# Optimization experiments

Hardware: AMD Instinct MI355X
Metric: run time of the kernel (lower is better)

The kernel has to match this reference:

```python
import jax, jax.numpy as jnp
import numpy as np

EPS = 1e-5

def layer_norm(x, gamma, beta):
    mu = jnp.mean(x, axis=-1, keepdims=True)
    var = jnp.mean(jnp.square(x - mu), axis=-1, keepdims=True)
    return (x - mu) * jax.lax.rsqrt(var + EPS) * gamma + beta

def setup_inputs() -> dict:
    key = jax.random.key(0)
    ks = jax.random.split(key, 12)
    B, N, F, H, K = 32, 2048, 128, 256, 64
    A_hat = jax.random.uniform(ks[0], (B, N, N), dtype=jnp.float32) / N  # row-normalized-ish adjacency
    X = jax.random.normal(ks[1], (B, N, F), dtype=jnp.float32)
    def lin(k, din, dout):
        s = 1.0 / np.sqrt(din)
        k1, k2 = jax.random.split(k)
        W = jax.random.uniform(k1, (din, dout), minval=-s, maxval=s, dtype=jnp.float32)
        b = jax.random.uniform(k2, (dout,), minval=-s, maxval=s, dtype=jnp.float32)
        return W, b
    W1, b1 = lin(ks[2], F, H)
    W2, b2 = lin(ks[3], H, H)
    Wa, ba = lin(ks[4], H, K)
    Wl, bl = lin(ks[5], H, K)
    g1 = jnp.ones((H,), jnp.float32); beta1 = jnp.zeros((H,), jnp.float32)
    g2 = jnp.ones((H,), jnp.float32); beta2 = jnp.zeros((H,), jnp.float32)
    return {"A_hat": A_hat, "X": X, "W1": W1, "b1": b1, "g1": g1, "beta1": beta1,
            "W2": W2, "b2": b2, "g2": g2, "beta2": beta2,
            "Wa": Wa, "ba": ba, "Wl": Wl, "bl": bl}

def reference(A_hat, X, W1, b1, g1, beta1, W2, b2, g2, beta2, Wa, ba, Wl, bl):
    # Layer 1: aggregate -> linear -> LayerNorm -> ReLU (dropout is eval identity)
    H = jnp.einsum('bnm,bmf->bnf', A_hat, X)
    H = jnp.einsum('bnf,fh->bnh', H, W1) + b1
    H = jax.nn.relu(layer_norm(H, g1, beta1))
    # Layer 2
    H = jnp.einsum('bnm,bmh->bnh', A_hat, H)
    H = jnp.einsum('bnh,hk->bnk', H, W2) + b2
    H = jax.nn.relu(layer_norm(H, g2, beta2))
    # mean readout over nodes
    g = jnp.mean(H, axis=1)
    pred_arr_reg = g @ Wa + ba
    logits = g @ Wl + bl
    return (pred_arr_reg, logits)
```

## Files before the change

kernel.cpp:

```cpp
#include <hip/hip_runtime.h>
#include <hip/hip_bf16.h>

#define NN 2048

typedef __attribute__((ext_vector_type(4))) float f32x4;
typedef __attribute__((ext_vector_type(8))) short bf16x8;

__device__ __forceinline__ unsigned short f2bf(float f) {
  __hip_bfloat16 h = __float2bfloat16(f);
  return __builtin_bit_cast(unsigned short, h);
}
__device__ __forceinline__ unsigned int pk2(float a, float b) {
  return (unsigned int)f2bf(a) | ((unsigned int)f2bf(b) << 16);
}
__device__ __forceinline__ void gld_lds16(const void* g, void* l) {
  __builtin_amdgcn_global_load_lds(
      (const __attribute__((address_space(1))) unsigned int*)g,
      (__attribute__((address_space(3))) unsigned int*)l, 16, 0, 0);
}

__global__ void k_tr_cvt(const float* __restrict__ src, unsigned short* __restrict__ dst,
                         int R, int C) {
  int b = blockIdx.z;
  src += (size_t)b * R * C;
  dst += (size_t)b * R * C;
  __shared__ float tile[32][33];
  int r0 = blockIdx.x * 32, c0 = blockIdx.y * 32;
  int t = threadIdx.x;
  int r = t >> 3, c4 = (t & 7) << 2;
  float4 v = *(const float4*)(src + (size_t)(r0 + r) * C + c0 + c4);
  tile[r][c4 + 0] = v.x; tile[r][c4 + 1] = v.y; tile[r][c4 + 2] = v.z; tile[r][c4 + 3] = v.w;
  __syncthreads();
  ushort4 o;
  o.x = f2bf(tile[c4 + 0][r]); o.y = f2bf(tile[c4 + 1][r]);
  o.z = f2bf(tile[c4 + 2][r]); o.w = f2bf(tile[c4 + 3][r]);
  *(ushort4*)(dst + (size_t)(c0 + r) * R + r0 + c4) = o;
}

#define AGG_STEP(KT, AREGC, AREGN, CUR)                                        \
  {                                                                            \
    const int kt_ = (KT);                                                      \
    if (kt_ < NKT - 2) {                 \
      const float* p_ = apb + (size_t)(kt_ + 2) * 64;                          \
      _Pragma("unroll") for (int j = 0; j < F4; ++j)                           \
          AREGN[j] = ((const float4*)p_)[j];                                   \
    }                                                                          \
    if (kt_ < NKT - 1) {                                                       \
      _Pragma("unroll") for (int i = 0; i < 4; ++i) {         \
        int jj = i * NT + t;                                                   \
        int n_ = jj >> 3, s_ = jj & 7, sp_ = s_ ^ (n_ & 7);                    \
        gld_lds16(BTb + (size_t)n_ * NN + (size_t)(kt_ + 1) * 64 + sp_ * 8,    \
                  &Bs[(CUR) ^ 1][(i * NT + wid * 64) * 8]);                    \
      }                                                                        \
      _Pragma("unroll") for (int i = 0; i < F4 / 2; ++i) {  \
        uint4 w_;                                                              \
        w_.x = pk2(AREGC[2 * i].x, AREGC[2 * i].y);                            \
        w_.y = pk2(AREGC[2 * i].z, AREGC[2 * i].w);                            \
        w_.z = pk2(AREGC[2 * i + 1].x, AREGC[2 * i + 1].y);                    \
        w_.w = pk2(AREGC[2 * i + 1].z, AREGC[2 * i + 1].w);                    \
        int s_ = ak * (F4 / 2) + i, sp_ = s_ ^ (ar & 7);                       \
        *(uint4*)&As[(CUR) ^ 1][(ar * 8 + sp_) * 8] = w_;                      \
      }                                                                        \
    }                                                                          \
    _Pragma("unroll") for (int kh = 0; kh < 2; ++kh) {                         \
      bf16x8 af[4], bfr[4];                                                    \
      _Pragma("unroll") for (int mi = 0; mi < 4; ++mi) {                       \
        int row = wr * 64 + mi * 16 + lr;                                      \
        int sp_ = (kh * 4 + q) ^ (row & 7);                                    \
        af[mi] = *(const bf16x8*)&As[CUR][(row * 8 + sp_) * 8];                \
      }                                                                        \
      _Pragma("unroll") for (int ni = 0; ni < 4; ++ni) {                       \
        int row = wc * 64 + ni * 16 + lr;                                      \
        int sp_ = (kh * 4 + q) ^ (row & 7);                                    \
        bfr[ni] = *(const bf16x8*)&Bs[CUR][(row * 8 + sp_) * 8];               \
      }                                                                        \
      _Pragma("unroll") for (int mi = 0; mi < 4; ++mi)                         \
        _Pragma("unroll") for (int ni = 0; ni < 4; ++ni)                       \
          acc[mi][ni] = __builtin_amdgcn_mfma_f32_16x16x32_bf16(               \
              af[mi], bfr[ni], acc[mi][ni], 0, 0, 0);                          \
    }                                                                          \
    __syncthreads();                                                           \
  }

template <int NCOLS>
__global__ __launch_bounds__(NCOLS * 2, 2) void k_agg(
    const float* __restrict__ A, const unsigned short* __restrict__ BT,
    unsigned short* __restrict__ C) {
  constexpr int NT = NCOLS * 2;
  constexpr int NWC = NCOLS / 64;
  constexpr int TPR = NT / 128;
  constexpr int FPT = 8192 / NT;
  constexpr int F4 = FPT / 4;
  constexpr int NKT = NN / 64;
  static_assert(NCOLS * 8 == NT * 4, "B gld count");

  __shared__ __align__(16) unsigned short As[2][128 * 64];
  __shared__ __align__(16) unsigned short Bs[2][NCOLS * 64];
  int b = blockIdx.z;
  const float* Ab = A + (size_t)b * NN * NN;
  const unsigned short* BTb = BT + (size_t)b * (size_t)NCOLS * NN;
  unsigned short* Cb = C + (size_t)b * NN * NCOLS;
  int m0 = blockIdx.x * 128;
  int t = threadIdx.x, lane = t & 63, wid = t >> 6;
  int wr = wid / NWC, wc = wid % NWC;
  int q = lane >> 4, lr = lane & 15;
  int ar = t / TPR, ak = t % TPR;
  const float* apb = Ab + (size_t)(m0 + ar) * NN + ak * FPT;

  f32x4 acc[4][4] = {};
  float4 aregA[F4], aregB[F4];

  {
#pragma unroll
    for (int j = 0; j < F4; ++j) aregA[j] = ((const float4*)apb)[j];
#pragma unroll
    for (int i = 0; i < 4; ++i) {
      int jj = i * NT + t;
      int n = jj >> 3, s = jj & 7, sp = s ^ (n & 7);
      gld_lds16(BTb + (size_t)n * NN + sp * 8, &Bs[0][(i * NT + wid * 64) * 8]);
    }
#pragma unroll
    for (int i = 0; i < F4 / 2; ++i) {
      uint4 w;
      w.x = pk2(aregA[2 * i].x, aregA[2 * i].y);
      w.y = pk2(aregA[2 * i].z, aregA[2 * i].w);
      w.z = pk2(aregA[2 * i + 1].x, aregA[2 * i + 1].y);
      w.w = pk2(aregA[2 * i + 1].z, aregA[2 * i + 1].w);
      int s = ak * (F4 / 2) + i, sp = s ^ (ar & 7);
      *(uint4*)&As[0][(ar * 8 + sp) * 8] = w;
    }
#pragma unroll
    for (int j = 0; j < F4; ++j) aregB[j] = ((const float4*)(apb + 64))[j];
  }
  __syncthreads();

  for (int k2 = 0; k2 < NKT / 2; ++k2) {
    AGG_STEP(2 * k2, aregB, aregA, 0);
    AGG_STEP(2 * k2 + 1, aregA, aregB, 1);
  }

#pragma unroll
  for (int mi = 0; mi < 4; ++mi) {
#pragma unroll
    for (int ni = 0; ni < 4; ++ni) {
#pragma unroll
      for (int j = 0; j < 4; ++j) {
        int row = m0 + wr * 64 + mi * 16 + q * 4 + j;
        int col = wc * 64 + ni * 16 + lr;
        Cb[(size_t)row * NCOLS + col] = f2bf(acc[mi][ni][j]);
      }
    }
  }
}

__global__ void k_lin_ln(const unsigned short* __restrict__ Hin, const unsigned short* __restrict__ WT,
                         const float* __restrict__ bias, const float* __restrict__ gamma,
                         const float* __restrict__ beta, int Fin,
                         unsigned short* __restrict__ HTout, float* __restrict__ gpart, int mode) {
  __shared__ __align__(16) unsigned short Ash[128 * 64];
  __shared__ __align__(16) unsigned short Wsh[256 * 64];
  __shared__ float red[2][128][4];
  int b = blockIdx.y, n0 = blockIdx.x * 128;
  const unsigned short* Hb = Hin + (size_t)b * NN * Fin;
  int t = threadIdx.x, lane = t & 63, wid = t >> 6;
  int wr = wid >> 2, wc = wid & 3;
  int q = lane >> 4, lr = lane & 15;
  f32x4 acc[4][4] = {};
  int nkt = Fin >> 6;
  for (int kt = 0; kt < nkt; ++kt) {
#pragma unroll
    for (int i = 0; i < 2; ++i) {
      int jj = i * 512 + t;
      int n = jj >> 3, s = jj & 7, sp = s ^ (n & 7);
      gld_lds16(Hb + (size_t)(n0 + n) * Fin + kt * 64 + sp * 8, &Ash[(i * 512 + wid * 64) * 8]);
    }
#pragma unroll
    for (int i = 0; i < 4; ++i) {
      int jj = i * 512 + t;
      int h = jj >> 3, s = jj & 7, sp = s ^ (h & 7);
      gld_lds16(WT + (size_t)h * Fin + kt * 64 + sp * 8, &Wsh[(i * 512 + wid * 64) * 8]);
    }
    __syncthreads();
#pragma unroll
    for (int kh = 0; kh < 2; ++kh) {
      bf16x8 af[4], wf[4];
#pragma unroll
      for (int mi = 0; mi < 4; ++mi) {
        int row = wr * 64 + mi * 16 + lr;
        int sp = (kh * 4 + q) ^ (row & 7);
        af[mi] = *(const bf16x8*)&Ash[(row * 8 + sp) * 8];
      }
#pragma unroll
      for (int ni = 0; ni < 4; ++ni) {
        int hrow = wc * 64 + ni * 16 + lr;
        int sp = (kh * 4 + q) ^ (hrow & 7);
        wf[ni] = *(const bf16x8*)&Wsh[(hrow * 8 + sp) * 8];
      }
#pragma unroll
      for (int mi = 0; mi < 4; ++mi) {
#pragma unroll
        for (int ni = 0; ni < 4; ++ni)
          acc[mi][ni] = __builtin_amdgcn_mfma_f32_16x16x32_bf16(af[mi], wf[ni], acc[mi][ni], 0, 0, 0);
      }
    }
    __syncthreads();
  }
  float bcol[4], gcol[4], zcol[4];
#pragma unroll
  for (int ni = 0; ni < 4; ++ni) {
    int col = wc * 64 + ni * 16 + lr;
    bcol[ni] = bias[col]; gcol[ni] = gamma[col]; zcol[ni] = beta[col];
  }
#pragma unroll
  for (int mi = 0; mi < 4; ++mi) {
#pragma unroll
    for (int j = 0; j < 4; ++j) {
      float s = 0.f, ss = 0.f;
#pragma unroll
      for (int ni = 0; ni < 4; ++ni) {
        float v = acc[mi][ni][j] + bcol[ni];
        acc[mi][ni][j] = v;
        s += v; ss += v * v;
      }
#pragma unroll
      for (int m = 1; m < 16; m <<= 1) { s += __shfl_xor(s, m); ss += __shfl_xor(ss, m); }
      if (lr == 0) {
        int rl = wr * 64 + mi * 16 + q * 4 + j;
        red[0][rl][wc] = s;
        red[1][rl][wc] = ss;
      }
    }
  }
  __syncthreads();
#pragma unroll
  for (int mi = 0; mi < 4; ++mi) {
#pragma unroll
    for (int j = 0; j < 4; ++j) {
      int rl = wr * 64 + mi * 16 + q * 4 + j;
      float s = red[0][rl][0] + red[0][rl][1] + red[0][rl][2] + red[0][rl][3];
      float ss = red[1][rl][0] + red[1][rl][1] + red[1][rl][2] + red[1][rl][3];
      float mean = s * (1.f / 256.f);
      float var = ss * (1.f / 256.f) - mean * mean;
      float inv = rsqrtf(var + 1e-5f);
#pragma unroll
      for (int ni = 0; ni < 4; ++ni) {
        float v = (acc[mi][ni][j] - mean) * inv * gcol[ni] + zcol[ni];
        acc[mi][ni][j] = v > 0.f ? v : 0.f;
      }
    }
  }
  if (mode == 0) {
#pragma unroll
    for (int mi = 0; mi < 4; ++mi) {
#pragma unroll
      for (int ni = 0; ni < 4; ++ni) {
        int col = wc * 64 + ni * 16 + lr;
        int rowb = n0 + wr * 64 + mi * 16 + q * 4;
        ushort4 o;
        o.x = f2bf(acc[mi][ni][0]); o.y = f2bf(acc[mi][ni][1]);
        o.z = f2bf(acc[mi][ni][2]); o.w = f2bf(acc[mi][ni][3]);
        *(ushort4*)(HTout + ((size_t)b * 256 + col) * NN + rowb) = o;
      }
    }
  } else {
#pragma unroll
    for (int ni = 0; ni < 4; ++ni) {
      float cs = 0.f;
#pragma unroll
      for (int mi = 0; mi < 4; ++mi) {
#pragma unroll
        for (int j = 0; j < 4; ++j) cs += acc[mi][ni][j];
      }
      cs += __shfl_xor(cs, 16);
      cs += __shfl_xor(cs, 32);
      if (q == 0) {
        int col = wc * 64 + ni * 16 + lr;
        gpart[(((size_t)b * 16 + blockIdx.x) * 2 + wr) * 256 + col] = cs;
      }
    }
  }
}

__global__ void k_readout(const float* __restrict__ gpart, const float* __restrict__ Wa,
                          const float* __restrict__ ba, const float* __restrict__ Wl,
                          const float* __restrict__ bl, float* __restrict__ out) {
  __shared__ float gl[256];
  int b = blockIdx.x, t = threadIdx.x;
  float s = 0.f;
#pragma unroll 4
  for (int p = 0; p < 32; ++p) s += gpart[((size_t)b * 32 + p) * 256 + t];
  gl[t] = s * (1.f / 2048.f);
  __syncthreads();
  if (t < 128) {
    int k = t & 63;
    const float* W = (t >= 64) ? Wl : Wa;
    const float* bb = (t >= 64) ? bl : ba;
    float a = 0.f;
    for (int h = 0; h < 256; ++h) a += gl[h] * W[h * 64 + k];
    a += bb[k];
    out[((t >= 64) ? 2048 : 0) + b * 64 + k] = a;
  }
}

extern "C" void kernel_launch(void* const* d_in, const int* in_sizes, int n_in,
                              void* d_out, int out_size, void* d_ws, size_t ws_size,
                              hipStream_t stream) {
  const float* A_hat = (const float*)d_in[0];
  const float* X   = (const float*)d_in[1];
  const float* W1  = (const float*)d_in[2];
  const float* b1  = (const float*)d_in[3];
  const float* g1  = (const float*)d_in[4];
  const float* be1 = (const float*)d_in[5];
  const float* W2  = (const float*)d_in[6];
  const float* b2  = (const float*)d_in[7];
  const float* g2  = (const float*)d_in[8];
  const float* be2 = (const float*)d_in[9];
  const float* Wa  = (const float*)d_in[10];
  const float* ba  = (const float*)d_in[11];
  const float* Wl  = (const float*)d_in[12];
  const float* bl  = (const float*)d_in[13];

  char* ws = (char*)d_ws;
  const size_t MB = 1024 * 1024;
  unsigned short* XT    = (unsigned short*)(ws);
  unsigned short* Hagg1 = (unsigned short*)(ws + 16 * MB);
  unsigned short* Hagg2 = (unsigned short*)(ws);
  unsigned short* H1T   = (unsigned short*)(ws + 32 * MB);
  unsigned short* W1T   = (unsigned short*)(ws + 64 * MB);
  unsigned short* W2T   = (unsigned short*)(ws + 64 * MB + 256 * 1024);
  float* gpart          = (float*)(ws + 65 * MB);

  k_tr_cvt<<<dim3(64, 4, 32), 256, 0, stream>>>(X, XT, 2048, 128);
  k_tr_cvt<<<dim3(4, 8, 1), 256, 0, stream>>>(W1, W1T, 128, 256);
  k_tr_cvt<<<dim3(8, 8, 1), 256, 0, stream>>>(W2, W2T, 256, 256);
  k_agg<128><<<dim3(16, 1, 32), 256, 0, stream>>>(A_hat, XT, Hagg1);
  k_lin_ln<<<dim3(16, 32), 512, 0, stream>>>(Hagg1, W1T, b1, g1, be1, 128, H1T, nullptr, 0);
  k_agg<256><<<dim3(16, 1, 32), 512, 0, stream>>>(A_hat, H1T, Hagg2);
  k_lin_ln<<<dim3(16, 32), 512, 0, stream>>>(Hagg2, W2T, b2, g2, be2, 256, nullptr, gpart, 1);
  k_readout<<<dim3(32), 256, 0, stream>>>(gpart, Wa, ba, Wl, bl, (float*)d_out);
}
```

Before: 390.0 us.

## Fuse aggregation GEMM with linear+LayerNorm+ReLU epilogue in one kernel

Merges k_agg and k_lin_ln into one templated kernel. Each block keeps its aggregated 128-row tile in LDS as bf16, reusing the A/B staging buffers, then runs the weight GEMM, LayerNorm and ReLU directly on it. This removes the global round trip of the intermediate Hagg buffers and two kernel launches. The layer-1 aggregation also moves from 256 to 512 threads with a different warp tiling, trading register and occupancy behaviour for the fusion.

```diff
diff --git a/kernel.cpp b/kernel.cpp
--- a/kernel.cpp
+++ b/kernel.cpp
@@ -40,97 +40,98 @@
 #define AGG_STEP(KT, AREGC, AREGN, CUR)                                        \
   {                                                                            \
     const int kt_ = (KT);                                                      \
-    if (kt_ < NKT - 2) {                 \
+    if (kt_ < NKT - 2) {                           \
       const float* p_ = apb + (size_t)(kt_ + 2) * 64;                          \
-      _Pragma("unroll") for (int j = 0; j < F4; ++j)                           \
+      _Pragma("unroll") for (int j = 0; j < 4; ++j)                            \
           AREGN[j] = ((const float4*)p_)[j];                                   \
     }                                                                          \
     if (kt_ < NKT - 1) {                                                       \
-      _Pragma("unroll") for (int i = 0; i < 4; ++i) {         \
-        int jj = i * NT + t;                                                   \
+      _Pragma("unroll") for (int i = 0; i < NF; ++i) {        \
+        int jj = i * 512 + t;                                                  \
         int n_ = jj >> 3, s_ = jj & 7, sp_ = s_ ^ (n_ & 7);                    \
         gld_lds16(BTb + (size_t)n_ * NN + (size_t)(kt_ + 1) * 64 + sp_ * 8,    \
-                  &Bs[(CUR) ^ 1][(i * NT + wid * 64) * 8]);                    \
+                  &Bs[(CUR) ^ 1][(i * 512 + wid * 64) * 8]);                   \
       }                                                                        \
-      _Pragma("unroll") for (int i = 0; i < F4 / 2; ++i) {  \
+      _Pragma("unroll") for (int i = 0; i < 2; ++i) {     \
         uint4 w_;                                                              \
         w_.x = pk2(AREGC[2 * i].x, AREGC[2 * i].y);                            \
         w_.y = pk2(AREGC[2 * i].z, AREGC[2 * i].w);                            \
         w_.z = pk2(AREGC[2 * i + 1].x, AREGC[2 * i + 1].y);                    \
         w_.w = pk2(AREGC[2 * i + 1].z, AREGC[2 * i + 1].w);                    \
-        int s_ = ak * (F4 / 2) + i, sp_ = s_ ^ (ar & 7);                       \
+        int s_ = ak * 2 + i, sp_ = s_ ^ (ar & 7);                              \
         *(uint4*)&As[(CUR) ^ 1][(ar * 8 + sp_) * 8] = w_;                      \
       }                                                                        \
     }                                                                          \
     _Pragma("unroll") for (int kh = 0; kh < 2; ++kh) {                         \
-      bf16x8 af[4], bfr[4];                                                    \
+      bf16x8 af[4], bfr[NF];                                                   \
       _Pragma("unroll") for (int mi = 0; mi < 4; ++mi) {                       \
         int row = wr * 64 + mi * 16 + lr;                                      \
         int sp_ = (kh * 4 + q) ^ (row & 7);                                    \
         af[mi] = *(const bf16x8*)&As[CUR][(row * 8 + sp_) * 8];                \
       }                                                                        \
-      _Pragma("unroll") for (int ni = 0; ni < 4; ++ni) {                       \
-        int row = wc * 64 + ni * 16 + lr;                                      \
-        int sp_ = (kh * 4 + q) ^ (row & 7);                                    \
-        bfr[ni] = *(const bf16x8*)&Bs[CUR][(row * 8 + sp_) * 8];               \
+      _Pragma("unroll") for (int ni = 0; ni < NF; ++ni) {                      \
+        int brow = wc * WN + ni * 16 + lr;                                     \
+        int sp_ = (kh * 4 + q) ^ (brow & 7);                                   \
+        bfr[ni] = *(const bf16x8*)&Bs[CUR][(brow * 8 + sp_) * 8];              \
       }                                                                        \
       _Pragma("unroll") for (int mi = 0; mi < 4; ++mi)                         \
-        _Pragma("unroll") for (int ni = 0; ni < 4; ++ni)                       \
+        _Pragma("unroll") for (int ni = 0; ni < NF; ++ni)                      \
           acc[mi][ni] = __builtin_amdgcn_mfma_f32_16x16x32_bf16(               \
               af[mi], bfr[ni], acc[mi][ni], 0, 0, 0);                          \
     }                                                                          \
     __syncthreads();                                                           \
   }
 
-template <int NCOLS>
-__global__ __launch_bounds__(NCOLS * 2, 2) void k_agg(
+template <int NCOLS, int MODE>
+__global__ __launch_bounds__(512, NCOLS == 128 ? 4 : 2) void k_agg_fused(
     const float* __restrict__ A, const unsigned short* __restrict__ BT,
-    unsigned short* __restrict__ C) {
-  constexpr int NT = NCOLS * 2;
-  constexpr int NWC = NCOLS / 64;
-  constexpr int TPR = NT / 128;
-  constexpr int FPT = 8192 / NT;
-  constexpr int F4 = FPT / 4;
+    const unsigned short* __restrict__ WT, const float* __restrict__ bias,
+    const float* __restrict__ gamma, const float* __restrict__ beta,
+    unsigned short* __restrict__ HTout, float* __restrict__ gpart) {
+  constexpr int WN = NCOLS / 4;
+  constexpr int NF = NCOLS / 64;
   constexpr int NKT = NN / 64;
-  static_assert(NCOLS * 8 == NT * 4, "B gld count");
+  constexpr int FIN = NCOLS;
+  constexpr int NQT = FIN / 64;
 
   __shared__ __align__(16) unsigned short As[2][128 * 64];
   __shared__ __align__(16) unsigned short Bs[2][NCOLS * 64];
+  __shared__ float red[2][128][4];
+
   int b = blockIdx.z;
   const float* Ab = A + (size_t)b * NN * NN;
   const unsigned short* BTb = BT + (size_t)b * (size_t)NCOLS * NN;
-  unsigned short* Cb = C + (size_t)b * NN * NCOLS;
   int m0 = blockIdx.x * 128;
   int t = threadIdx.x, lane = t & 63, wid = t >> 6;
-  int wr = wid / NWC, wc = wid % NWC;
+  int wr = wid >> 2, wc = wid & 3;
   int q = lane >> 4, lr = lane & 15;
-  int ar = t / TPR, ak = t % TPR;
-  const float* apb = Ab + (size_t)(m0 + ar) * NN + ak * FPT;
-
-  f32x4 acc[4][4] = {};
-  float4 aregA[F4], aregB[F4];
+  int ar = t >> 2, ak = t & 3;
+  const float* apb = Ab + (size_t)(m0 + ar) * NN + ak * 16;
+
+  f32x4 acc[4][NF] = {};
+  float4 aregA[4], aregB[4];
 
   {
 #pragma unroll
-    for (int j = 0; j < F4; ++j) aregA[j] = ((const float4*)apb)[j];
-#pragma unroll
-    for (int i = 0; i < 4; ++i) {
-      int jj = i * NT + t;
+    for (int j = 0; j < 4; ++j) aregA[j] = ((const float4*)apb)[j];
+#pragma unroll
+    for (int i = 0; i < NF; ++i) {
+      int jj = i * 512 + t;
       int n = jj >> 3, s = jj & 7, sp = s ^ (n & 7);
-      gld_lds16(BTb + (size_t)n * NN + sp * 8, &Bs[0][(i * NT + wid * 64) * 8]);
-    }
-#pragma unroll
-    for (int i = 0; i < F4 / 2; ++i) {
+      gld_lds16(BTb + (size_t)n * NN + sp * 8, &Bs[0][(i * 512 + wid * 64) * 8]);
+    }
+#pragma unroll
+    for (int i = 0; i < 2; ++i) {
       uint4 w;
       w.x = pk2(aregA[2 * i].x, aregA[2 * i].y);
       w.y = pk2(aregA[2 * i].z, aregA[2 * i].w);
       w.z = pk2(aregA[2 * i + 1].x, aregA[2 * i + 1].y);
       w.w = pk2(aregA[2 * i + 1].z, aregA[2 * i + 1].w);
-      int s = ak * (F4 / 2) + i, sp = s ^ (ar & 7);
+      int s = ak * 2 + i, sp = s ^ (ar & 7);
       *(uint4*)&As[0][(ar * 8 + sp) * 8] = w;
     }
 #pragma unroll
-    for (int j = 0; j < F4; ++j) aregB[j] = ((const float4*)(apb + 64))[j];
+    for (int j = 0; j < 4; ++j) aregB[j] = ((const float4*)(apb + 64))[j];
   }
   __syncthreads();
 
@@ -139,72 +140,57 @@
     AGG_STEP(2 * k2 + 1, aregA, aregB, 1);
   }
 
+  unsigned short* Hs = (NCOLS == 128) ? &As[0][0] : &Bs[0][0];
+  unsigned short* Ws = (NCOLS == 128) ? &Bs[0][0] : &As[0][0];
 #pragma unroll
   for (int mi = 0; mi < 4; ++mi) {
 #pragma unroll
-    for (int ni = 0; ni < 4; ++ni) {
+    for (int ni = 0; ni < NF; ++ni) {
 #pragma unroll
       for (int j = 0; j < 4; ++j) {
-        int row = m0 + wr * 64 + mi * 16 + q * 4 + j;
-        int col = wc * 64 + ni * 16 + lr;
-        Cb[(size_t)row * NCOLS + col] = f2bf(acc[mi][ni][j]);
-      }
-    }
-  }
-}
-
-__global__ void k_lin_ln(const unsigned short* __restrict__ Hin, const unsigned short* __restrict__ WT,
-                         const float* __restrict__ bias, const float* __restrict__ gamma,
-                         const float* __restrict__ beta, int Fin,
-                         unsigned short* __restrict__ HTout, float* __restrict__ gpart, int mode) {
-  __shared__ __align__(16) unsigned short Ash[128 * 64];
-  __shared__ __align__(16) unsigned short Wsh[256 * 64];
-  __shared__ float red[2][128][4];
-  int b = blockIdx.y, n0 = blockIdx.x * 128;
-  const unsigned short* Hb = Hin + (size_t)b * NN * Fin;
-  int t = threadIdx.x, lane = t & 63, wid = t >> 6;
-  int wr = wid >> 2, wc = wid & 3;
-  int q = lane >> 4, lr = lane & 15;
-  f32x4 acc[4][4] = {};
-  int nkt = Fin >> 6;
-  for (int kt = 0; kt < nkt; ++kt) {
-#pragma unroll
-    for (int i = 0; i < 2; ++i) {
-      int jj = i * 512 + t;
-      int n = jj >> 3, s = jj & 7, sp = s ^ (n & 7);
-      gld_lds16(Hb + (size_t)(n0 + n) * Fin + kt * 64 + sp * 8, &Ash[(i * 512 + wid * 64) * 8]);
-    }
+        int row = wr * 64 + mi * 16 + q * 4 + j;
+        int col = wc * WN + ni * 16 + lr;
+        int sp = (col >> 3) ^ (row & 7);
+        Hs[row * FIN + sp * 8 + (col & 7)] = f2bf(acc[mi][ni][j]);
+      }
+    }
+  }
+
+  f32x4 acc2[4][4] = {};
+  for (int qt = 0; qt < NQT; ++qt) {
+    __syncthreads();
 #pragma unroll
     for (int i = 0; i < 4; ++i) {
       int jj = i * 512 + t;
       int h = jj >> 3, s = jj & 7, sp = s ^ (h & 7);
-      gld_lds16(WT + (size_t)h * Fin + kt * 64 + sp * 8, &Wsh[(i * 512 + wid * 64) * 8]);
+      gld_lds16(WT + (size_t)h * FIN + qt * 64 + sp * 8, Ws + (i * 512 + wid * 64) * 8);
     }
     __syncthreads();
 #pragma unroll
     for (int kh = 0; kh < 2; ++kh) {
-      bf16x8 af[4], wf[4];
+      bf16x8 hf[4], wf[4];
 #pragma unroll
       for (int mi = 0; mi < 4; ++mi) {
         int row = wr * 64 + mi * 16 + lr;
-        int sp = (kh * 4 + q) ^ (row & 7);
-        af[mi] = *(const bf16x8*)&Ash[(row * 8 + sp) * 8];
+        int slot = qt * 8 + kh * 4 + q;
+        int sp = slot ^ (row & 7);
+        hf[mi] = *(const bf16x8*)&Hs[row * FIN + sp * 8];
       }
 #pragma unroll
       for (int ni = 0; ni < 4; ++ni) {
-        int hrow = wc * 64 + ni * 16 + lr;
-        int sp = (kh * 4 + q) ^ (hrow & 7);
-        wf[ni] = *(const bf16x8*)&Wsh[(hrow * 8 + sp) * 8];
+        int h = wc * 64 + ni * 16 + lr;
+        int sp = (kh * 4 + q) ^ (h & 7);
+        wf[ni] = *(const bf16x8*)&Ws[(h * 8 + sp) * 8];
       }
 #pragma unroll
       for (int mi = 0; mi < 4; ++mi) {
 #pragma unroll
         for (int ni = 0; ni < 4; ++ni)
-          acc[mi][ni] = __builtin_amdgcn_mfma_f32_16x16x32_bf16(af[mi], wf[ni], acc[mi][ni], 0, 0, 0);
-      }
-    }
-    __syncthreads();
-  }
+          acc2[mi][ni] = __builtin_amdgcn_mfma_f32_16x16x32_bf16(hf[mi], wf[ni], acc2[mi][ni], 0, 0, 0);
+      }
+    }
+  }
+
   float bcol[4], gcol[4], zcol[4];
 #pragma unroll
   for (int ni = 0; ni < 4; ++ni) {
@@ -218,8 +204,8 @@
       float s = 0.f, ss = 0.f;
 #pragma unroll
       for (int ni = 0; ni < 4; ++ni) {
-        float v = acc[mi][ni][j] + bcol[ni];
-        acc[mi][ni][j] = v;
+        float v = acc2[mi][ni][j] + bcol[ni];
+        acc2[mi][ni][j] = v;
         s += v; ss += v * v;
       }
 #pragma unroll
@@ -244,21 +230,21 @@
       float inv = rsqrtf(var + 1e-5f);
 #pragma unroll
       for (int ni = 0; ni < 4; ++ni) {
-        float v = (acc[mi][ni][j] - mean) * inv * gcol[ni] + zcol[ni];
-        acc[mi][ni][j] = v > 0.f ? v : 0.f;
-      }
-    }
-  }
-  if (mode == 0) {
+        float v = (acc2[mi][ni][j] - mean) * inv * gcol[ni] + zcol[ni];
+        acc2[mi][ni][j] = v > 0.f ? v : 0.f;
+      }
+    }
+  }
+  if (MODE == 0) {
 #pragma unroll
     for (int mi = 0; mi < 4; ++mi) {
 #pragma unroll
       for (int ni = 0; ni < 4; ++ni) {
         int col = wc * 64 + ni * 16 + lr;
-        int rowb = n0 + wr * 64 + mi * 16 + q * 4;
+        int rowb = m0 + wr * 64 + mi * 16 + q * 4;
         ushort4 o;
-        o.x = f2bf(acc[mi][ni][0]); o.y = f2bf(acc[mi][ni][1]);
-        o.z = f2bf(acc[mi][ni][2]); o.w = f2bf(acc[mi][ni][3]);
+        o.x = f2bf(acc2[mi][ni][0]); o.y = f2bf(acc2[mi][ni][1]);
+        o.z = f2bf(acc2[mi][ni][2]); o.w = f2bf(acc2[mi][ni][3]);
         *(ushort4*)(HTout + ((size_t)b * 256 + col) * NN + rowb) = o;
       }
     }
@@ -269,7 +255,7 @@
 #pragma unroll
       for (int mi = 0; mi < 4; ++mi) {
 #pragma unroll
-        for (int j = 0; j < 4; ++j) cs += acc[mi][ni][j];
+        for (int j = 0; j < 4; ++j) cs += acc2[mi][ni][j];
       }
       cs += __shfl_xor(cs, 16);
       cs += __shfl_xor(cs, 32);
@@ -322,20 +308,18 @@
 
   char* ws = (char*)d_ws;
   const size_t MB = 1024 * 1024;
-  unsigned short* XT    = (unsigned short*)(ws);
-  unsigned short* Hagg1 = (unsigned short*)(ws + 16 * MB);
-  unsigned short* Hagg2 = (unsigned short*)(ws);
-  unsigned short* H1T   = (unsigned short*)(ws + 32 * MB);
-  unsigned short* W1T   = (unsigned short*)(ws + 64 * MB);
-  unsigned short* W2T   = (unsigned short*)(ws + 64 * MB + 256 * 1024);
-  float* gpart          = (float*)(ws + 65 * MB);
+  unsigned short* XT  = (unsigned short*)(ws);
+  unsigned short* H1T = (unsigned short*)(ws + 16 * MB);
+  unsigned short* W1T = (unsigned short*)(ws + 48 * MB);
+  unsigned short* W2T = (unsigned short*)(ws + 48 * MB + 256 * 1024);
+  float* gpart        = (float*)(ws + 49 * MB);
 
   k_tr_cvt<<<dim3(64, 4, 32), 256, 0, stream>>>(X, XT, 2048, 128);
   k_tr_cvt<<<dim3(4, 8, 1), 256, 0, stream>>>(W1, W1T, 128, 256);
   k_tr_cvt<<<dim3(8, 8, 1), 256, 0, stream>>>(W2, W2T, 256, 256);
-  k_agg<128><<<dim3(16, 1, 32), 256, 0, stream>>>(A_hat, XT, Hagg1);
-  k_lin_ln<<<dim3(16, 32), 512, 0, stream>>>(Hagg1, W1T, b1, g1, be1, 128, H1T, nullptr, 0);
-  k_agg<256><<<dim3(16, 1, 32), 512, 0, stream>>>(A_hat, H1T, Hagg2);
-  k_lin_ln<<<dim3(16, 32), 512, 0, stream>>>(Hagg2, W2T, b2, g2, be2, 256, nullptr, gpart, 1);
+  k_agg_fused<128, 0><<<dim3(16, 1, 32), 512, 0, stream>>>(
+      A_hat, XT, W1T, b1, g1, be1, H1T, nullptr);
+  k_agg_fused<256, 1><<<dim3(16, 1, 32), 512, 0, stream>>>(
+      A_hat, H1T, W2T, b2, g2, be2, nullptr, gpart);
   k_readout<<<dim3(32), 256, 0, stream>>>(gpart, Wa, ba, Wl, bl, (float*)d_out);
 }
```

After: 338.0 us. 13.3% less time.
